# Kernel tuning notes

Hardware: AMD Instinct MI355X
Metric: run time of the kernel (lower is better)

Reference implementation:

```python
import jax, jax.numpy as jnp
import numpy as np

B, S, P, D = 32, 512, 512, 768

def setup_inputs() -> dict:
    key = jax.random.key(0)
    k1, k2 = jax.random.split(key)
    inputs = jax.random.normal(k1, (B, S, D), dtype=jnp.float32)
    prototypes = jax.random.normal(k2, (P, D), dtype=jnp.float32)
    return {"inputs": inputs, "prototypes": prototypes}

def reference(inputs, prototypes):
    # Squared Euclidean distance from every token vector to every prototype:
    # but the cross term is a GEMM and the huge [B,S,P,D] intermediate is never built).
    x_sq = jnp.sum(inputs * inputs, axis=-1, keepdims=True)          # [B, S, 1]
    p_sq = jnp.sum(prototypes * prototypes, axis=-1)                 # [P]
    cross = jnp.einsum('bsd,pd->bsp', inputs, prototypes)            # [B, S, P]
    distances = x_sq + p_sq[None, None, :] - 2.0 * cross             # [B, S, P]
    return (distances, prototypes)
```

## Files before the change

kernel.cpp:

```cpp
#include <hip/hip_runtime.h>
#include <hip/hip_bf16.h>


#define M_TOK 16384
#define N_PROT 512
#define K_DIM 768
#define BK 32
#define NCH (K_DIM / BK)
#define ASTR (K_DIM + 8)

typedef __attribute__((ext_vector_type(4))) float f32x4;
typedef __attribute__((ext_vector_type(8))) short bf16x8;

__device__ inline unsigned short f2bf(float f) {
    unsigned int u = __float_as_uint(f);
    u += 0x7fffu + ((u >> 16) & 1u);
    return (unsigned short)(u >> 16);
}

__global__ __launch_bounds__(256) void prep_b(
    const float* __restrict__ p,
    unsigned short* __restrict__ b_bf, float* __restrict__ p_sq,
    float* __restrict__ proto_out)
{
    const int row  = blockIdx.x * 4 + (threadIdx.x >> 6);
    const int lane = threadIdx.x & 63;

    const float4* src4 = (const float4*)(p + (size_t)row * K_DIM);
    unsigned short* dst = b_bf + (size_t)row * K_DIM;
    float4* pout4 = (float4*)(proto_out + (size_t)row * K_DIM);

    float ssum = 0.0f;
#pragma unroll
    for (int j = 0; j < 3; ++j) {
        const int idx = lane + j * 64;
        float4 v = src4[idx];
        ssum += v.x * v.x + v.y * v.y + v.z * v.z + v.w * v.w;
        ushort4 b;
        b.x = f2bf(v.x); b.y = f2bf(v.y); b.z = f2bf(v.z); b.w = f2bf(v.w);
        ((ushort4*)dst)[idx] = b;
        pout4[idx] = v;
    }
#pragma unroll
    for (int off = 32; off > 0; off >>= 1) ssum += __shfl_down(ssum, off);
    if (lane == 0) p_sq[row] = ssum;
}

__global__ __launch_bounds__(512, 2) void dist_main(
    const float* __restrict__ X,
    const unsigned short* __restrict__ Bb,
    const float* __restrict__ p_sq,
    float* __restrict__ out)
{
    __shared__ unsigned short lds_a[64 * ASTR];
    __shared__ float lds_xsq[64];

    const int tid  = threadIdx.x;
    const int wave = tid >> 6;
    const int lane = tid & 63;
    const int bm   = blockIdx.x << 6;
    const int wn   = wave << 6;
    const int quad = lane >> 4;
    const int l16  = lane & 15;

    const int ar = tid >> 3;
    const int ac = tid & 7;
    const float* aptr = X + (size_t)(bm + ar) * K_DIM;
    float asq = 0.0f;
#pragma unroll
    for (int j = 0; j < 24; ++j) {
        const int c4 = ac + 8 * j;
        float4 v = *(const float4*)(aptr + (size_t)c4 * 4);
        asq += v.x * v.x + v.y * v.y + v.z * v.z + v.w * v.w;
        ushort4 u;
        u.x = f2bf(v.x); u.y = f2bf(v.y); u.z = f2bf(v.z); u.w = f2bf(v.w);
        *(ushort4*)&lds_a[ar * ASTR + c4 * 4] = u;
    }
#pragma unroll
    for (int off = 1; off < 8; off <<= 1) asq += __shfl_xor(asq, off);
    if (ac == 0) lds_xsq[ar] = asq;

    __syncthreads();

    const f32x4 zero = {0.0f, 0.0f, 0.0f, 0.0f};
    f32x4 acc[4][4];
#pragma unroll
    for (int mt = 0; mt < 4; ++mt)
#pragma unroll
        for (int nt = 0; nt < 4; ++nt) acc[mt][nt] = zero;

    const unsigned short* bp = Bb + (size_t)(wn + l16) * K_DIM + quad * 8;

    bf16x8 bcur[4], bnxt[4];
#pragma unroll
    for (int nt = 0; nt < 4; ++nt)
        bcur[nt] = *(const bf16x8*)(bp + (size_t)(nt * 16) * K_DIM);

    for (int kc = 0; kc < NCH; ++kc) {
        const int k0 = kc * BK;
        if (kc + 1 < NCH) {
#pragma unroll
            for (int nt = 0; nt < 4; ++nt)
                bnxt[nt] = *(const bf16x8*)(bp + (size_t)(nt * 16) * K_DIM + k0 + BK);
        }

        bf16x8 af[4];
#pragma unroll
        for (int mt = 0; mt < 4; ++mt)
            af[mt] = *(const bf16x8*)&lds_a[(mt * 16 + l16) * ASTR + k0 + quad * 8];

#pragma unroll
        for (int mt = 0; mt < 4; ++mt)
#pragma unroll
            for (int nt = 0; nt < 4; ++nt)
                acc[mt][nt] = __builtin_amdgcn_mfma_f32_16x16x32_bf16(
                    af[mt], bcur[nt], acc[mt][nt], 0, 0, 0);

#pragma unroll
        for (int nt = 0; nt < 4; ++nt) bcur[nt] = bnxt[nt];
    }

    float ps[4];
#pragma unroll
    for (int nt = 0; nt < 4; ++nt) ps[nt] = p_sq[wn + nt * 16 + l16];

#pragma unroll
    for (int mt = 0; mt < 4; ++mt) {
#pragma unroll
        for (int i = 0; i < 4; ++i) {
            const int lr = mt * 16 + quad * 4 + i;
            const float xs = lds_xsq[lr];
            float* orow = out + (size_t)(bm + lr) * N_PROT + wn + l16;
#pragma unroll
            for (int nt = 0; nt < 4; ++nt)
                orow[nt * 16] = xs + ps[nt] - 2.0f * acc[mt][nt][i];
        }
    }
}

extern "C" void kernel_launch(void* const* d_in, const int* in_sizes, int n_in,
                              void* d_out, int out_size, void* d_ws, size_t ws_size,
                              hipStream_t stream) {
    const float* inputs = (const float*)d_in[0];
    const float* protos = (const float*)d_in[1];
    float* out = (float*)d_out;
    float* proto_out = out + (size_t)M_TOK * N_PROT;

    char* ws = (char*)d_ws;
    unsigned short* b_bf = (unsigned short*)ws;
    float* p_sq = (float*)(ws + 786432);

    prep_b<<<128, 256, 0, stream>>>(protos, b_bf, p_sq, proto_out);
    dist_main<<<M_TOK / 64, 512, 0, stream>>>(inputs, b_bf, p_sq, out);
}
```

Measured before the change: 116.0 us.

## Split N across two blocks and double-buffer A tile in LDS by K chunks

```diff
diff --git a/kernel.cpp b/kernel.cpp
--- a/kernel.cpp
+++ b/kernel.cpp
@@ -5,9 +5,10 @@
 #define M_TOK 16384
 #define N_PROT 512
 #define K_DIM 768
-#define BK 32
-#define NCH (K_DIM / BK)
-#define ASTR (K_DIM + 8)
+#define BKC 128
+#define NKC (K_DIM / BKC)
+#define NSK (K_DIM / 32)
+#define ASTR 136
 
 typedef __attribute__((ext_vector_type(4))) float f32x4;
 typedef __attribute__((ext_vector_type(8))) short bf16x8;
@@ -46,83 +47,122 @@
     if (lane == 0) p_sq[row] = ssum;
 }
 
-__global__ __launch_bounds__(512, 2) void dist_main(
+__global__ __launch_bounds__(512, 4) void dist_main(
     const float* __restrict__ X,
     const unsigned short* __restrict__ Bb,
     const float* __restrict__ p_sq,
     float* __restrict__ out)
 {
-    __shared__ unsigned short lds_a[64 * ASTR];
+    __shared__ unsigned short lds_a[2][64 * ASTR];
     __shared__ float lds_xsq[64];
+
+    const int bid     = blockIdx.x;
+    const int logical = (bid & 7) * 64 + (bid >> 3);
+    const int ms = logical >> 1;
+    const int nh = logical & 1;
+    const int bm = ms << 6;
+    const int bn = nh << 8;
 
     const int tid  = threadIdx.x;
     const int wave = tid >> 6;
     const int lane = tid & 63;
-    const int bm   = blockIdx.x << 6;
-    const int wn   = wave << 6;
+    const int wn   = bn + (wave << 5);
     const int quad = lane >> 4;
     const int l16  = lane & 15;
 
     const int ar = tid >> 3;
     const int ac = tid & 7;
-    const float* aptr = X + (size_t)(bm + ar) * K_DIM;
+    const float* aptr = X + (size_t)(bm + ar) * K_DIM + ac * 4;
+
     float asq = 0.0f;
+
+    {
+        float4 v0 = *(const float4*)(aptr);
+        float4 v1 = *(const float4*)(aptr + 32);
+        float4 v2 = *(const float4*)(aptr + 64);
+        float4 v3 = *(const float4*)(aptr + 96);
+        float4 vv[4] = {v0, v1, v2, v3};
 #pragma unroll
-    for (int j = 0; j < 24; ++j) {
-        const int c4 = ac + 8 * j;
-        float4 v = *(const float4*)(aptr + (size_t)c4 * 4);
-        asq += v.x * v.x + v.y * v.y + v.z * v.z + v.w * v.w;
-        ushort4 u;
-        u.x = f2bf(v.x); u.y = f2bf(v.y); u.z = f2bf(v.z); u.w = f2bf(v.w);
-        *(ushort4*)&lds_a[ar * ASTR + c4 * 4] = u;
+        for (int j = 0; j < 4; ++j) {
+            float4 v = vv[j];
+            asq += v.x * v.x + v.y * v.y + v.z * v.z + v.w * v.w;
+            ushort4 u;
+            u.x = f2bf(v.x); u.y = f2bf(v.y); u.z = f2bf(v.z); u.w = f2bf(v.w);
+            *(ushort4*)&lds_a[0][ar * ASTR + (ac + 8 * j) * 4] = u;
+        }
     }
+    __syncthreads();
+
+    const unsigned short* bp = Bb + (size_t)(wn + l16) * K_DIM + quad * 8;
+
+    bf16x8 bcur0 = *(const bf16x8*)(bp);
+    bf16x8 bcur1 = *(const bf16x8*)(bp + 16 * K_DIM);
+    bf16x8 bnxt0, bnxt1;
+
+    const f32x4 zero = {0.0f, 0.0f, 0.0f, 0.0f};
+    f32x4 acc[4][2];
+#pragma unroll
+    for (int mt = 0; mt < 4; ++mt) {
+        acc[mt][0] = zero; acc[mt][1] = zero;
+    }
+
+    for (int kc = 0; kc < NKC; ++kc) {
+        float4 s0, s1, s2, s3;
+        if (kc + 1 < NKC) {
+            const float* ap = aptr + (kc + 1) * BKC;
+            s0 = *(const float4*)(ap);
+            s1 = *(const float4*)(ap + 32);
+            s2 = *(const float4*)(ap + 64);
+            s3 = *(const float4*)(ap + 96);
+        }
+
+#pragma unroll
+        for (int s = 0; s < 4; ++s) {
+            const int kk = kc * 4 + s;
+            if (kk + 1 < NSK) {
+                const int kn = (kk + 1) * 32;
+                bnxt0 = *(const bf16x8*)(bp + kn);
+                bnxt1 = *(const bf16x8*)(bp + 16 * K_DIM + kn);
+            }
+
+            bf16x8 af[4];
+#pragma unroll
+            for (int mt = 0; mt < 4; ++mt)
+                af[mt] = *(const bf16x8*)&lds_a[kc & 1]
+                    [(mt * 16 + l16) * ASTR + s * 32 + quad * 8];
+
+#pragma unroll
+            for (int mt = 0; mt < 4; ++mt) {
+                acc[mt][0] = __builtin_amdgcn_mfma_f32_16x16x32_bf16(
+                    af[mt], bcur0, acc[mt][0], 0, 0, 0);
+                acc[mt][1] = __builtin_amdgcn_mfma_f32_16x16x32_bf16(
+                    af[mt], bcur1, acc[mt][1], 0, 0, 0);
+            }
+            bcur0 = bnxt0; bcur1 = bnxt1;
+        }
+
+        if (kc + 1 < NKC) {
+            unsigned short* aw = &lds_a[(kc + 1) & 1][ar * ASTR + ac * 4];
+            float4 vv[4] = {s0, s1, s2, s3};
+#pragma unroll
+            for (int j = 0; j < 4; ++j) {
+                float4 v = vv[j];
+                asq += v.x * v.x + v.y * v.y + v.z * v.z + v.w * v.w;
+                ushort4 u;
+                u.x = f2bf(v.x); u.y = f2bf(v.y); u.z = f2bf(v.z); u.w = f2bf(v.w);
+                *(ushort4*)(aw + 8 * j * 4) = u;
+            }
+        }
+        __syncthreads();
+    }
+
 #pragma unroll
     for (int off = 1; off < 8; off <<= 1) asq += __shfl_xor(asq, off);
     if (ac == 0) lds_xsq[ar] = asq;
-
     __syncthreads();
 
-    const f32x4 zero = {0.0f, 0.0f, 0.0f, 0.0f};
-    f32x4 acc[4][4];
-#pragma unroll
-    for (int mt = 0; mt < 4; ++mt)
-#pragma unroll
-        for (int nt = 0; nt < 4; ++nt) acc[mt][nt] = zero;
-
-    const unsigned short* bp = Bb + (size_t)(wn + l16) * K_DIM + quad * 8;
-
-    bf16x8 bcur[4], bnxt[4];
-#pragma unroll
-    for (int nt = 0; nt < 4; ++nt)
-        bcur[nt] = *(const bf16x8*)(bp + (size_t)(nt * 16) * K_DIM);
-
-    for (int kc = 0; kc < NCH; ++kc) {
-        const int k0 = kc * BK;
-        if (kc + 1 < NCH) {
-#pragma unroll
-            for (int nt = 0; nt < 4; ++nt)
-                bnxt[nt] = *(const bf16x8*)(bp + (size_t)(nt * 16) * K_DIM + k0 + BK);
-        }
-
-        bf16x8 af[4];
-#pragma unroll
-        for (int mt = 0; mt < 4; ++mt)
-            af[mt] = *(const bf16x8*)&lds_a[(mt * 16 + l16) * ASTR + k0 + quad * 8];
-
-#pragma unroll
-        for (int mt = 0; mt < 4; ++mt)
-#pragma unroll
-            for (int nt = 0; nt < 4; ++nt)
-                acc[mt][nt] = __builtin_amdgcn_mfma_f32_16x16x32_bf16(
-                    af[mt], bcur[nt], acc[mt][nt], 0, 0, 0);
-
-#pragma unroll
-        for (int nt = 0; nt < 4; ++nt) bcur[nt] = bnxt[nt];
-    }
-
-    float ps[4];
-#pragma unroll
-    for (int nt = 0; nt < 4; ++nt) ps[nt] = p_sq[wn + nt * 16 + l16];
+    float ps0 = p_sq[wn + l16];
+    float ps1 = p_sq[wn + 16 + l16];
 
 #pragma unroll
     for (int mt = 0; mt < 4; ++mt) {
@@ -131,9 +171,8 @@
             const int lr = mt * 16 + quad * 4 + i;
             const float xs = lds_xsq[lr];
             float* orow = out + (size_t)(bm + lr) * N_PROT + wn + l16;
-#pragma unroll
-            for (int nt = 0; nt < 4; ++nt)
-                orow[nt * 16] = xs + ps[nt] - 2.0f * acc[mt][nt][i];
+            orow[0]  = xs + ps0 - 2.0f * acc[mt][0][i];
+            orow[16] = xs + ps1 - 2.0f * acc[mt][1][i];
         }
     }
 }
@@ -151,5 +190,5 @@
     float* p_sq = (float*)(ws + 786432);
 
     prep_b<<<128, 256, 0, stream>>>(protos, b_bf, p_sq, proto_out);
-    dist_main<<<M_TOK / 64, 512, 0, stream>>>(inputs, b_bf, p_sq, out);
+    dist_main<<<2 * (M_TOK / 64), 512, 0, stream>>>(inputs, b_bf, p_sq, out);
 }
```

Result: slower. 121.7 us (+5.0%).
